# Optimization experiments

Hardware: AMD Instinct MI355X
Metric: run time of the kernel (lower is better)

Reference implementation:

```python
import jax, jax.numpy as jnp
from jax import lax
import numpy as np

IMG = 1024.0

def setup_inputs() -> dict:
    key = jax.random.key(0)
    k1, k2, k3, k4 = jax.random.split(key, 4)
    B, N, M = 128, 2000, 200
    # build valid boxes: [x1, y1, x2, y2] with x2 > x1, y2 > y1
    pxy = jax.random.uniform(k1, (B, N, 2), jnp.float32, 0.0, IMG - 130.0)
    pwh = jax.random.uniform(k2, (B, N, 2), jnp.float32, 10.0, 120.0)
    gxy = jax.random.uniform(k3, (B, M, 2), jnp.float32, 0.0, IMG - 130.0)
    gwh = jax.random.uniform(k4, (B, M, 2), jnp.float32, 10.0, 120.0)
    pred_boxes = jnp.concatenate([pxy, pxy + pwh], axis=-1)
    gt_boxes = jnp.concatenate([gxy, gxy + gwh], axis=-1)
    return {"pred_boxes": pred_boxes, "gt_boxes": gt_boxes}


def _box_iou(b1, b2):
    # b1: [N,4], b2: [M,4] -> iou [N,M]
    area1 = (b1[:, 2] - b1[:, 0]) * (b1[:, 3] - b1[:, 1])
    area2 = (b2[:, 2] - b2[:, 0]) * (b2[:, 3] - b2[:, 1])
    lt = jnp.maximum(b1[:, None, :2], b2[None, :, :2])
    rb = jnp.minimum(b1[:, None, 2:], b2[None, :, 2:])
    wh = jnp.clip(rb - lt, 0.0)
    inter = wh[..., 0] * wh[..., 1]
    union = area1[:, None] + area2[None, :] - inter
    return inter / union


def _greedy_precision(iou, threshold):
    # iou: [N,M]; sequential greedy matching over pred rows
    M = iou.shape[1]
    col_ids = jnp.arange(M)

    def step(carry, row):
        matched, fp = carry  # matched: [M] bool, fp: scalar float
        masked = jnp.where(matched, -1.0, row)
        idx = jnp.argmax(masked)
        hit = masked[idx] >= threshold
        matched = matched | (hit & (col_ids == idx))
        fp = fp + jnp.where(hit, 0.0, 1.0)
        return (matched, fp), None

    init = (jnp.zeros((M,), bool), jnp.float32(0.0))
    (matched, fp), _ = lax.scan(step, init, iou)
    tp = matched.sum().astype(iou.dtype)
    fn = jnp.float32(M) - tp  # unmatched gt columns (iou >= 0 > -1)
    return tp / (tp + fp + fn)


def reference(pred_boxes, gt_boxes):
    # pred_boxes: [B,N,4], gt_boxes: [B,M,4]
    thresholds = jnp.asarray(np.arange(0.5, 0.75, 0.05), jnp.float32)  # 5 thresholds
    ious = jax.vmap(_box_iou)(pred_boxes, gt_boxes)  # [B,N,M]
    per_img = jax.vmap(
        lambda iou: jax.vmap(lambda t: _greedy_precision(iou, t))(thresholds).mean()
    )(ious)  # [B]
    return per_img.mean()
```

## Files before the change

### kernel.cpp

```cpp
#include <hip/hip_runtime.h>
#include <cstdint>

#pragma clang fp contract(off)

#define NROWS 2000
#define MCOLS 200
#define BIMG  128
#define NTHR  5
#define NPMAX 1024
#define GB    8
#define NCELL (GB * GB)
#define PCHUNK 250
#define NCHUNK (NROWS / PCHUNK)
#define SCAP  96

#define CFAC 0.33302208f

typedef unsigned long long ull;

__global__ void __launch_bounds__(256) screen_kernel(
        const float4* __restrict__ pred, const float4* __restrict__ gt,
        ull* __restrict__ entries, int* __restrict__ blkcnt,
        int* __restrict__ done_images) {
    __shared__ float gx[MCOLS], gy[MCOLS], gz[MCOLS], gw[MCOLS], ga2[MCOLS];
    __shared__ int   gid_l[MCOLS];
    __shared__ int   goff_l[NCELL + 1];
    __shared__ int   gcur[NCELL];
    __shared__ int   lcnt;
    const int b = blockIdx.y, tid = threadIdx.x;

    if (blockIdx.x == 0 && b == 0 && tid == 0) *done_images = 0;

    const int r = blockIdx.x * PCHUNK + (tid < PCHUNK ? tid : PCHUNK - 1);
    const float4 p = pred[(size_t)b * NROWS + r];

    if (tid < NCELL) gcur[tid] = 0;
    if (tid == 0) lcnt = 0;
    __syncthreads();

    float4 gr = make_float4(0.f, 0.f, 0.f, 0.f);
    int gbn = -1;
    if (tid < MCOLS) {
        gr = gt[(size_t)b * MCOLS + tid];
        int cx = (int)gr.x >> 7, cy = (int)gr.y >> 7;
        cx = cx < 0 ? 0 : (cx > GB - 1 ? GB - 1 : cx);
        cy = cy < 0 ? 0 : (cy > GB - 1 ? GB - 1 : cy);
        gbn = cy * GB + cx;
        atomicAdd(&gcur[gbn], 1);
    }
    __syncthreads();

    if (tid < 64) {
        const int v = gcur[tid];
        int inc = v;
#pragma unroll
        for (int off = 1; off < 64; off <<= 1) {
            const int u = __shfl_up(inc, off);
            if (tid >= off) inc += u;
        }
        goff_l[tid + 1] = inc;
        if (tid == 0) goff_l[0] = 0;
        gcur[tid] = inc - v;
    }
    __syncthreads();

    if (gbn >= 0) {
        const int idx = atomicAdd(&gcur[gbn], 1);
        gx[idx] = gr.x; gy[idx] = gr.y; gz[idx] = gr.z; gw[idx] = gr.w;
        ga2[idx] = (gr.z - gr.x) * (gr.w - gr.y);
        gid_l[idx] = tid;
    }
    __syncthreads();

    ull* __restrict__ slice = entries + (size_t)(b * NCHUNK + blockIdx.x) * SCAP;
    if (tid < PCHUNK) {
        const float a1 = (p.z - p.x) * (p.w - p.y);
        const float ca1 = CFAC * a1;
        int cx = (int)p.x >> 7, cy = (int)p.y >> 7;
        cx = cx < 0 ? 0 : (cx > GB - 1 ? GB - 1 : cx);
        cy = cy < 0 ? 0 : (cy > GB - 1 ? GB - 1 : cy);
        const int xlo = cx > 0 ? cx - 1 : 0;
        const int xhi = cx < GB - 1 ? cx + 1 : GB - 1;
        const int ylo = cy > 0 ? cy - 1 : 0;
        const int yhi = cy < GB - 1 ? cy + 1 : GB - 1;
        for (int gyy = ylo; gyy <= yhi; ++gyy) {
            const int lo = goff_l[gyy * GB + xlo];
            const int hi = goff_l[gyy * GB + xhi + 1];
            for (int j = lo; j < hi; ++j) {
                const float a2 = ga2[j];
                const float ltx = fmaxf(p.x, gx[j]), lty = fmaxf(p.y, gy[j]);
                const float rbx = fminf(p.z, gz[j]), rby = fminf(p.w, gw[j]);
                const float wx = fmaxf(rbx - ltx, 0.0f), wy = fmaxf(rby - lty, 0.0f);
                const float inter = wx * wy;
                if (inter >= ca1 + CFAC * a2) {
                    const float uni = (a1 + a2) - inter;
                    const float iou = inter / uni;
                    const int idx = atomicAdd(&lcnt, 1);
                    if (idx < SCAP)
                        slice[idx] = ((ull)r << 40)
                            | ((ull)(__float_as_uint(iou) ^ 0xFFFFFFFFu) << 8)
                            | (ull)gid_l[j];
                }
            }
        }
    }
    __syncthreads();
    if (tid == 0) blkcnt[b * NCHUNK + blockIdx.x] = min(lcnt, SCAP);
}

__global__ void __launch_bounds__(256) match_kernel(
        const ull* __restrict__ entries, const int* __restrict__ blkcnt,
        int* __restrict__ done_images, float* __restrict__ perimg,
        float* __restrict__ out) {
    __shared__ ull   keys[NPMAX];
    __shared__ int   base[NCHUNK + 1];
    __shared__ float precs[NTHR];
    __shared__ int   flag;
    const int b = blockIdx.x;
    const int tid = threadIdx.x;

    if (tid == 0) {
        int s = 0;
#pragma unroll
        for (int c = 0; c < NCHUNK; ++c) {
            base[c] = s;
            s += blkcnt[b * NCHUNK + c];
        }
        base[NCHUNK] = s;
    }
    __syncthreads();
    const int n = base[NCHUNK];

#pragma unroll
    for (int c = 0; c < NCHUNK; ++c) {
        const int lo = base[c], cnt = base[c + 1] - lo;
        for (int i = tid; i < cnt; i += 256)
            keys[lo + i] = entries[(size_t)(b * NCHUNK + c) * SCAP + i];
    }
    int np = 64;
    while (np < n) np <<= 1;
    for (int i = tid; i < np; i += 256)
        if (i >= n) keys[i] = ~0ull;
    __syncthreads();

    for (int k = 2; k <= np; k <<= 1) {
        for (int j = k >> 1; j > 0; j >>= 1) {
            for (int i = tid; i < np; i += 256) {
                const int ixj = i ^ j;
                if (ixj > i) {
                    const ull a = keys[i], c = keys[ixj];
                    if ((a > c) == ((i & k) == 0)) { keys[i] = c; keys[ixj] = a; }
                }
            }
            __syncthreads();
        }
    }

    if (tid < NTHR) {
        const float thr = (float)(0.5 + 0.05 * (double)tid);
        const uint thr_inv = __float_as_uint(thr) ^ 0xFFFFFFFFu;
        ull m0 = 0, m1 = 0, m2 = 0, m3 = 0;
        int tp = 0, cur = -1;
        bool done = false;
#pragma unroll 4
        for (int e = 0; e < n; ++e) {
            const ull key = keys[e];
            const int row = (int)(key >> 40);
            const int col = (int)(key & 0xFFull);
            const uint ib  = (uint)(key >> 8);
            const bool newrow = (row != cur);
            cur = row;
            const bool undecided = newrow || !done;
            const int w = col >> 6;
            const ull bit = 1ull << (col & 63);
            const ull mm = (w == 0) ? m0 : (w == 1) ? m1 : (w == 2) ? m2 : m3;
            const bool decide = undecided && ((mm & bit) == 0);
            const bool hit = decide && (ib <= thr_inv);
            tp += hit ? 1 : 0;
            const ull sb = hit ? bit : 0ull;
            m0 |= (w == 0) ? sb : 0ull;
            m1 |= (w == 1) ? sb : 0ull;
            m2 |= (w == 2) ? sb : 0ull;
            m3 |= (w == 3) ? sb : 0ull;
            done = decide || (done && !newrow);
        }
        precs[tid] = (float)tp / (float)(NROWS + MCOLS - tp);
    }
    __syncthreads();
    if (tid == 0) {
        float s = 0.0f;
#pragma unroll
        for (int t = 0; t < NTHR; ++t) s += precs[t];
        __hip_atomic_store(&perimg[b], s / (float)NTHR,
                           __ATOMIC_RELAXED, __HIP_MEMORY_SCOPE_AGENT);
    }

    __syncthreads();
    __threadfence();
    if (tid == 0)
        flag = (atomicAdd(done_images, 1) == BIMG - 1) ? 1 : 0;
    __syncthreads();
    if (!flag) return;
    __threadfence();

    if (tid < 64) {
        const float v0 = __hip_atomic_load(&perimg[tid],
                           __ATOMIC_RELAXED, __HIP_MEMORY_SCOPE_AGENT);
        const float v1 = __hip_atomic_load(&perimg[tid + 64],
                           __ATOMIC_RELAXED, __HIP_MEMORY_SCOPE_AGENT);
        float s = v0 + v1;
#pragma unroll
        for (int off = 32; off; off >>= 1) s += __shfl_xor(s, off);
        if (tid == 0) out[0] = s / (float)BIMG;
    }
}

extern "C" void kernel_launch(void* const* d_in, const int* in_sizes, int n_in,
                              void* d_out, int out_size, void* d_ws, size_t ws_size,
                              hipStream_t stream) {
    const float4* pred = (const float4*)d_in[0];
    const float4* gt   = (const float4*)d_in[1];
    float* out = (float*)d_out;

    int*   doneim  = (int*)d_ws;
    int*   blkcnt  = doneim + 64;
    float* perimg  = (float*)(blkcnt + BIMG * NCHUNK);
    ull*   entries = (ull*)((char*)d_ws + 8192);

    screen_kernel<<<dim3(NCHUNK, BIMG), dim3(256), 0, stream>>>(
        pred, gt, entries, blkcnt, doneim);

    match_kernel<<<dim3(BIMG), dim3(256), 0, stream>>>(
        entries, blkcnt, doneim, perimg, out);
}
```

Measured before the change: 53.36 us.

## Fuse screen and match kernels via per-image last-block-done counter

Merges the screening and matching kernels into one launch. The last chunk block to finish for each image, detected with an acq_rel atomic counter, performs the sort and greedy match, so the second kernel launch and the grid-wide dependency between them go away. It also packs the gt boxes into float2 shared arrays and adds a hipMemsetAsync to reset the counters. Risks: the memset adds a small operation, shared memory per block grows with the keys array (possibly lowering occupancy for the screening phase), and the matching work now runs on whichever block finishes last.

```diff
diff --git a/kernel.cpp b/kernel.cpp
--- a/kernel.cpp
+++ b/kernel.cpp
@@ -18,18 +18,25 @@
 
 typedef unsigned long long ull;
 
-__global__ void __launch_bounds__(256) screen_kernel(
+#define ST_REL(p, v)  __hip_atomic_store((p), (v), __ATOMIC_RELAXED, __HIP_MEMORY_SCOPE_AGENT)
+#define LD_RLX(p)     __hip_atomic_load((p), __ATOMIC_RELAXED, __HIP_MEMORY_SCOPE_AGENT)
+
+__global__ void __launch_bounds__(256) fused_kernel(
         const float4* __restrict__ pred, const float4* __restrict__ gt,
         ull* __restrict__ entries, int* __restrict__ blkcnt,
-        int* __restrict__ done_images) {
-    __shared__ float gx[MCOLS], gy[MCOLS], gz[MCOLS], gw[MCOLS], ga2[MCOLS];
-    __shared__ int   gid_l[MCOLS];
-    __shared__ int   goff_l[NCELL + 1];
-    __shared__ int   gcur[NCELL];
-    __shared__ int   lcnt;
+        int* __restrict__ done_blocks, int* __restrict__ done_images,
+        float* __restrict__ perimg, float* __restrict__ out) {
+    __shared__ float2 g01[MCOLS], g23[MCOLS];
+    __shared__ float  ga2[MCOLS];
+    __shared__ int    gid_l[MCOLS];
+    __shared__ int    goff_l[NCELL + 1];
+    __shared__ int    gcur[NCELL];
+    __shared__ int    lcnt;
+    __shared__ ull    keys[NPMAX];
+    __shared__ int    base[NCHUNK + 1];
+    __shared__ float  precs[NTHR];
+    __shared__ int    flag;
     const int b = blockIdx.y, tid = threadIdx.x;
-
-    if (blockIdx.x == 0 && b == 0 && tid == 0) *done_images = 0;
 
     const int r = blockIdx.x * PCHUNK + (tid < PCHUNK ? tid : PCHUNK - 1);
     const float4 p = pred[(size_t)b * NROWS + r];
@@ -66,7 +73,8 @@
 
     if (gbn >= 0) {
         const int idx = atomicAdd(&gcur[gbn], 1);
-        gx[idx] = gr.x; gy[idx] = gr.y; gz[idx] = gr.z; gw[idx] = gr.w;
+        g01[idx] = make_float2(gr.x, gr.y);
+        g23[idx] = make_float2(gr.z, gr.w);
         ga2[idx] = (gr.z - gr.x) * (gr.w - gr.y);
         gid_l[idx] = tid;
     }
@@ -87,9 +95,10 @@
             const int lo = goff_l[gyy * GB + xlo];
             const int hi = goff_l[gyy * GB + xhi + 1];
             for (int j = lo; j < hi; ++j) {
+                const float2 gA = g01[j], gB = g23[j];
                 const float a2 = ga2[j];
-                const float ltx = fmaxf(p.x, gx[j]), lty = fmaxf(p.y, gy[j]);
-                const float rbx = fminf(p.z, gz[j]), rby = fminf(p.w, gw[j]);
+                const float ltx = fmaxf(p.x, gA.x), lty = fmaxf(p.y, gA.y);
+                const float rbx = fminf(p.z, gB.x), rby = fminf(p.w, gB.y);
                 const float wx = fmaxf(rbx - ltx, 0.0f), wy = fmaxf(rby - lty, 0.0f);
                 const float inter = wx * wy;
                 if (inter >= ca1 + CFAC * a2) {
@@ -97,34 +106,28 @@
                     const float iou = inter / uni;
                     const int idx = atomicAdd(&lcnt, 1);
                     if (idx < SCAP)
-                        slice[idx] = ((ull)r << 40)
+                        ST_REL(&slice[idx], ((ull)r << 40)
                             | ((ull)(__float_as_uint(iou) ^ 0xFFFFFFFFu) << 8)
-                            | (ull)gid_l[j];
+                            | (ull)gid_l[j]);
                 }
             }
         }
     }
     __syncthreads();
-    if (tid == 0) blkcnt[b * NCHUNK + blockIdx.x] = min(lcnt, SCAP);
-}
-
-__global__ void __launch_bounds__(256) match_kernel(
-        const ull* __restrict__ entries, const int* __restrict__ blkcnt,
-        int* __restrict__ done_images, float* __restrict__ perimg,
-        float* __restrict__ out) {
-    __shared__ ull   keys[NPMAX];
-    __shared__ int   base[NCHUNK + 1];
-    __shared__ float precs[NTHR];
-    __shared__ int   flag;
-    const int b = blockIdx.x;
-    const int tid = threadIdx.x;
+    if (tid == 0) {
+        ST_REL(&blkcnt[b * NCHUNK + blockIdx.x], min(lcnt, SCAP));
+        flag = (__hip_atomic_fetch_add(&done_blocks[b], 1, __ATOMIC_ACQ_REL,
+                __HIP_MEMORY_SCOPE_AGENT) == NCHUNK - 1) ? 1 : 0;
+    }
+    __syncthreads();
+    if (!flag) return;
 
     if (tid == 0) {
         int s = 0;
 #pragma unroll
         for (int c = 0; c < NCHUNK; ++c) {
             base[c] = s;
-            s += blkcnt[b * NCHUNK + c];
+            s += LD_RLX(&blkcnt[b * NCHUNK + c]);
         }
         base[NCHUNK] = s;
     }
@@ -135,7 +138,7 @@
     for (int c = 0; c < NCHUNK; ++c) {
         const int lo = base[c], cnt = base[c + 1] - lo;
         for (int i = tid; i < cnt; i += 256)
-            keys[lo + i] = entries[(size_t)(b * NCHUNK + c) * SCAP + i];
+            keys[lo + i] = LD_RLX(&entries[(size_t)(b * NCHUNK + c) * SCAP + i]);
     }
     int np = 64;
     while (np < n) np <<= 1;
@@ -191,23 +194,16 @@
         float s = 0.0f;
 #pragma unroll
         for (int t = 0; t < NTHR; ++t) s += precs[t];
-        __hip_atomic_store(&perimg[b], s / (float)NTHR,
-                           __ATOMIC_RELAXED, __HIP_MEMORY_SCOPE_AGENT);
-    }
-
-    __syncthreads();
-    __threadfence();
-    if (tid == 0)
-        flag = (atomicAdd(done_images, 1) == BIMG - 1) ? 1 : 0;
+        ST_REL(&perimg[b], s / (float)NTHR);
+        flag = (__hip_atomic_fetch_add(done_images, 1, __ATOMIC_ACQ_REL,
+                __HIP_MEMORY_SCOPE_AGENT) == BIMG - 1) ? 1 : 0;
+    }
     __syncthreads();
     if (!flag) return;
-    __threadfence();
 
     if (tid < 64) {
-        const float v0 = __hip_atomic_load(&perimg[tid],
-                           __ATOMIC_RELAXED, __HIP_MEMORY_SCOPE_AGENT);
-        const float v1 = __hip_atomic_load(&perimg[tid + 64],
-                           __ATOMIC_RELAXED, __HIP_MEMORY_SCOPE_AGENT);
+        const float v0 = LD_RLX(&perimg[tid]);
+        const float v1 = LD_RLX(&perimg[tid + 64]);
         float s = v0 + v1;
 #pragma unroll
         for (int off = 32; off; off >>= 1) s += __shfl_xor(s, off);
@@ -222,14 +218,14 @@
     const float4* gt   = (const float4*)d_in[1];
     float* out = (float*)d_out;
 
-    int*   doneim  = (int*)d_ws;
-    int*   blkcnt  = doneim + 64;
+    int*   donebl  = (int*)d_ws;
+    int*   doneim  = donebl + BIMG;
+    int*   blkcnt  = donebl + 256;
     float* perimg  = (float*)(blkcnt + BIMG * NCHUNK);
-    ull*   entries = (ull*)((char*)d_ws + 8192);
-
-    screen_kernel<<<dim3(NCHUNK, BIMG), dim3(256), 0, stream>>>(
-        pred, gt, entries, blkcnt, doneim);
-
-    match_kernel<<<dim3(BIMG), dim3(256), 0, stream>>>(
-        entries, blkcnt, doneim, perimg, out);
+    ull*   entries = (ull*)((char*)d_ws + 16384);
+
+    (void)hipMemsetAsync(donebl, 0, (BIMG + 1) * sizeof(int), stream);
+
+    fused_kernel<<<dim3(NCHUNK, BIMG), dim3(256), 0, stream>>>(
+        pred, gt, entries, blkcnt, donebl, doneim, perimg, out);
 }
```

Measured after the change: 75.84 us. 42.1% more time.
